# Kernel tuning notes

Measured on AMD Instinct MI355X. Metric: run time of the kernel, lower is better.

The kernel has to match this reference:

```python
import jax, jax.numpy as jnp
import numpy as np

DIM = 1024
NUM_HEADS = 16
HEAD_DIM = DIM // NUM_HEADS           # 64
WIDTH_SCALE = 0.5                      # set via configure_width in the source
CUR_HD = int(HEAD_DIM * WIDTH_SCALE)   # 32
CUR_DIM = CUR_HD * NUM_HEADS           # 512
SCALE = (HEAD_DIM ** -0.5) / (WIDTH_SCALE ** 0.5)
B, N = 2, 2048


def setup_inputs() -> dict:
    key = jax.random.key(0)
    k1, k2, k3 = jax.random.split(key, 3)
    x = jax.random.normal(k1, (B, N, DIM), dtype=jnp.float32)
    # 0.02 init keeps pre-softmax logits in a realistic range
    w_qkv = jax.random.normal(k2, (3 * DIM, DIM), dtype=jnp.float32) * 0.02
    w_proj = jax.random.normal(k3, (DIM, DIM), dtype=jnp.float32) * 0.02
    b_proj = jnp.zeros((DIM,), dtype=jnp.float32)
    return {"x": x, "w_qkv": w_qkv, "w_proj": w_proj, "b_proj": b_proj}


def reference(x, w_qkv, w_proj, b_proj):
    Bb, Nn, C = x.shape
    cq = 3 * CUR_DIM
    # dynamic-width slice of the fused QKV weight (qkv_bias=False)
    qkv = x @ w_qkv[:cq, :].T                              # (B, N, 3*CUR_DIM)
    qkv = qkv.reshape(Bb, Nn, 3, NUM_HEADS, CUR_HD).transpose(2, 0, 3, 1, 4)
    q, k, v = qkv[0], qkv[1], qkv[2]                       # (B, H, N, hd)
    attn = jax.nn.softmax(jnp.einsum('bhnd,bhmd->bhnm', q, k) * SCALE, axis=-1)
    o = jnp.einsum('bhnm,bhmd->bhnd', attn, v)             # (B, H, N, hd)
    o = o.transpose(0, 2, 1, 3).reshape(Bb, Nn, CUR_DIM)
    # proj uses only its first CUR_DIM input columns
    return o @ w_proj[:, :CUR_DIM].T + b_proj
```

## Files before the change

kernel.cpp:

```cpp
#include <hip/hip_runtime.h>

typedef __bf16 bf16;
typedef __bf16 bf16x8 __attribute__((ext_vector_type(8)));
typedef __bf16 bf16x4 __attribute__((ext_vector_type(4)));
typedef __bf16 bf16x2 __attribute__((ext_vector_type(2)));
typedef float  f32x4  __attribute__((ext_vector_type(4)));
typedef float  f32x16 __attribute__((ext_vector_type(16)));
typedef unsigned int uint32;

constexpr int DIM_  = 1024;
constexpr int NH    = 16;
constexpr int CHD   = 32;
constexpr int CDIM  = 512;
constexpr int CQ    = 1536;
constexpr int NSEQ  = 2048;
constexpr int M_    = 4096;
constexpr float ATT_SCALE = 0.17677669529663687f;
constexpr float QS_LOG2 = ATT_SCALE * 1.4426950408889634f;

__device__ inline void gload16(const bf16* g, bf16* l) {
    __builtin_amdgcn_global_load_lds((const __attribute__((address_space(1))) void*)g,
                                     (__attribute__((address_space(3))) void*)l, 16, 0, 0);
}

constexpr int NX4 = M_ * DIM_ / 4;
constexpr int NW4 = CQ * DIM_ / 4;
constexpr int NP4 = DIM_ * (CDIM / 4);
__global__ void cast_fused(const float* __restrict__ x, const float* __restrict__ wq,
                           const float* __restrict__ wp, bf16* __restrict__ xb,
                           bf16* __restrict__ wqb, bf16* __restrict__ wpb) {
    int i = blockIdx.x * blockDim.x + threadIdx.x;
    const float4* src;
    bf16x4* dst;
    if (i < NX4) {
        src = reinterpret_cast<const float4*>(x) + i;
        dst = reinterpret_cast<bf16x4*>(xb) + i;
    } else if (i < NX4 + NW4) {
        int j = i - NX4;
        src = reinterpret_cast<const float4*>(wq) + j;
        dst = reinterpret_cast<bf16x4*>(wqb) + j;
    } else {
        int j = i - (NX4 + NW4);
        int c = j >> 7, j4 = j & 127;
        src = reinterpret_cast<const float4*>(wp + c * DIM_) + j4;
        dst = reinterpret_cast<bf16x4*>(wpb + c * CDIM) + j4;
    }
    float4 v = *src;
    bf16x4 o = { (bf16)v.x, (bf16)v.y, (bf16)v.z, (bf16)v.w };
    *dst = o;
}

template<int KDIM, int MODE>
__launch_bounds__(256)
__global__ void gemm_nt(const bf16* __restrict__ A, const bf16* __restrict__ Bm,
                        bf16* __restrict__ qbo, bf16* __restrict__ kbo, bf16* __restrict__ vto,
                        float* __restrict__ Cf, const float* __restrict__ bias) {
    __shared__ __align__(16) bf16 SMEM[18432];
    bf16* As = SMEM;
    bf16* Bs = SMEM + 12288;
    const int tid = threadIdx.x;
    const int w = tid >> 6, lane = tid & 63;
    const int m0 = blockIdx.x * 128, n0 = blockIdx.y * 64;
    const int wr = (w >> 1) * 64, wc = (w & 1) * 32;
    const int lrow = lane >> 2, lk = (lane & 3) * 8;
    const int cl = lane & 15, gk8 = (lane >> 4) * 8;

    const bf16* ga = A  + (m0 + w * 16 + lrow) * KDIM + lk;
    const bf16* gb = Bm + (n0 + w * 16 + lrow) * KDIM + lk;

    constexpr int KT = KDIM / 32;

    auto stage = [&](int kt, int b) {
        gload16(ga + kt * 32,             As + b * 4096 + w * 512);
        gload16(ga + kt * 32 + 64 * KDIM, As + b * 4096 + 2048 + w * 512);
        gload16(gb + kt * 32,             Bs + b * 2048 + w * 512);
    };
    stage(0, 0);
    stage(1, 1);

    f32x4 acc[4][2] = {};

    for (int kt = 0; kt < KT; ++kt) {
        if (kt < KT - 1) asm volatile("s_waitcnt vmcnt(3)" ::: "memory");
        else             asm volatile("s_waitcnt vmcnt(0)" ::: "memory");
        __builtin_amdgcn_s_barrier();
        __builtin_amdgcn_sched_barrier(0);
        if (kt + 2 < KT) stage(kt + 2, (kt + 2) % 3);

        const bf16* as = As + (kt % 3) * 4096;
        const bf16* bs = Bs + (kt % 3) * 2048;
        bf16x8 af[4], bfr[2];
#pragma unroll
        for (int i = 0; i < 4; ++i)
            af[i]  = *reinterpret_cast<const bf16x8*>(as + (wr + i * 16 + cl) * 32 + gk8);
#pragma unroll
        for (int j = 0; j < 2; ++j)
            bfr[j] = *reinterpret_cast<const bf16x8*>(bs + (wc + j * 16 + cl) * 32 + gk8);
#pragma unroll
        for (int i = 0; i < 4; ++i)
#pragma unroll
            for (int j = 0; j < 2; ++j)
                acc[i][j] = __builtin_amdgcn_mfma_f32_16x16x32_bf16(af[i], bfr[j], acc[i][j], 0, 0, 0);
    }

    const int rg = (lane >> 4) * 4;
    if constexpr (MODE == 2) {
#pragma unroll
        for (int i = 0; i < 4; ++i)
#pragma unroll
            for (int j = 0; j < 2; ++j) {
                const int row = m0 + wr + i * 16 + rg;
                const int col = n0 + wc + j * 16 + cl;
                const float bv = bias[col];
#pragma unroll
                for (int r = 0; r < 4; ++r)
                    Cf[(row + r) * DIM_ + col] = acc[i][j][r] + bv;
            }
    } else {
        const int sec = n0 >> 9;
        if (sec == 2) {
#pragma unroll
            for (int i = 0; i < 4; ++i)
#pragma unroll
                for (int j = 0; j < 2; ++j) {
                    const int row = m0 + wr + i * 16 + rg;
                    const int col = n0 + wc + j * 16 + cl;
                    const int rem = col & 511;
                    const int h = rem >> 5, d = rem & 31;
                    const int bb = row >> 11, pos = row & 2047;
                    const int bh = bb * NH + h;
                    bf16x4 st;
#pragma unroll
                    for (int r = 0; r < 4; ++r) st[r] = (bf16)acc[i][j][r];
                    *reinterpret_cast<bf16x4*>(vto + (bh * CHD + d) * NSEQ + pos) = st;
                }
        } else {
            const float sc = sec ? 1.0f : QS_LOG2;
            __syncthreads();
#pragma unroll
            for (int i = 0; i < 4; ++i)
#pragma unroll
                for (int j = 0; j < 2; ++j)
#pragma unroll
                    for (int r = 0; r < 4; ++r)
                        SMEM[(wr + i * 16 + rg + r) * 72 + wc + j * 16 + cl] =
                            (bf16)(acc[i][j][r] * sc);
            __syncthreads();
            const int row = tid >> 1, ch = (tid & 1) * 32;
            const int m = m0 + row, bb = m >> 11, pos = m & 2047;
            const int col0 = n0 + ch;
            const int h = (col0 & 511) >> 5;
            bf16* dst = (sec ? kbo : qbo) + ((bb * NH + h) * NSEQ + pos) * CHD;
#pragma unroll
            for (int v4 = 0; v4 < 4; ++v4)
                *reinterpret_cast<bf16x8*>(dst + v4 * 8) =
                    *reinterpret_cast<const bf16x8*>(SMEM + row * 72 + ch + v4 * 8);
        }
    }
}

__device__ inline uint32 pkbf(float lo, float hi) {
    bf16x2 t = { (bf16)lo, (bf16)hi };
    return __builtin_bit_cast(uint32, t);
}

__launch_bounds__(512, 4)
__global__ void flash_kernel(const bf16* __restrict__ qb, const bf16* __restrict__ kb,
                             const bf16* __restrict__ vt, bf16* __restrict__ outb) {
    __shared__ __align__(16) char smem[32768];
    const int tid = threadIdx.x;
    const int w = tid >> 6, lane = tid & 63;
    const int lq = lane & 31, hi = lane >> 5;
    const int p = w & 3, half = w >> 2;

    const int blin = blockIdx.x;
    const int xcd = blin & 7, within = blin >> 3;
    const int head = xcd * 4 + (within >> 4);
    const int qblk = within & 15;
    const int q0 = qblk * 128 + p * 32;

    const bf16* Q = qb + head * (NSEQ * CHD);
    const bf16* K = kb + head * (NSEQ * CHD);
    const bf16* V = vt + head * (CHD * NSEQ);

    const bf16x8 qf0 = *reinterpret_cast<const bf16x8*>(Q + (q0 + lq) * CHD + hi * 8);
    const bf16x8 qf1 = *reinterpret_cast<const bf16x8*>(Q + (q0 + lq) * CHD + 16 + hi * 8);

    char* base = smem + half * 16384;
    const int sh = p >> 1, skc = p & 1;
    const bf16* srcK = K + (half * 1024 + sh * 32 + lq) * CHD + skc * 16 + hi * 8;
    const bf16* srcV = V + lq * NSEQ + half * 1024 + p * 16 + hi * 8;

    auto stage = [&](int t) {
        char* b = base + (t & 1) * 8192;
        gload16(srcK + t * 64 * CHD, (bf16*)(b + p * 1024));
        gload16(srcV + t * 64,       (bf16*)(b + 4096 + p * 1024));
    };
    stage(0);
    __syncthreads();

    f32x16 o = {};
    float rs[4] = {};
    const f32x16 zero16 = {};

    for (int t = 0; t < 16; ++t) {
        if (t < 15) stage(t + 1);
        char* buf = base + (t & 1) * 8192;
#pragma unroll
        for (int h = 0; h < 2; ++h) {
            const bf16x8 k0 = *reinterpret_cast<const bf16x8*>(buf + (h * 2 + 0) * 1024 + lane * 16);
            const bf16x8 k1 = *reinterpret_cast<const bf16x8*>(buf + (h * 2 + 1) * 1024 + lane * 16);
            __builtin_amdgcn_s_setprio(1);
            f32x16 s = __builtin_amdgcn_mfma_f32_32x32x16_bf16(k0, qf0, zero16, 0, 0, 0);
            s = __builtin_amdgcn_mfma_f32_32x32x16_bf16(k1, qf1, s, 0, 0, 0);
            __builtin_amdgcn_s_setprio(0);

#pragma unroll
            for (int r = 0; r < 16; ++r) s[r] = __builtin_amdgcn_exp2f(s[r]);
#pragma unroll
            for (int r = 0; r < 16; ++r) rs[r & 3] += s[r];

#pragma unroll
            for (int cc = 0; cc < 2; ++cc) {
                const int b8 = cc * 8;
                uint32 u0 = pkbf(s[b8 + 0], s[b8 + 1]);
                uint32 u1 = pkbf(s[b8 + 2], s[b8 + 3]);
                uint32 u2 = pkbf(s[b8 + 4], s[b8 + 5]);
                uint32 u3 = pkbf(s[b8 + 6], s[b8 + 7]);
                asm volatile("v_permlane32_swap_b32 %0, %1" : "+v"(u0), "+v"(u2));
                asm volatile("v_permlane32_swap_b32 %0, %1" : "+v"(u1), "+v"(u3));
                union { uint32 u[4]; bf16x8 v; } pb;
                pb.u[0] = u0; pb.u[1] = u1; pb.u[2] = u2; pb.u[3] = u3;
                const bf16x8 vf = *reinterpret_cast<const bf16x8*>(buf + 4096 + (h * 2 + cc) * 1024 + lane * 16);
                __builtin_amdgcn_s_setprio(1);
                o = __builtin_amdgcn_mfma_f32_32x32x16_bf16(vf, pb.v, o, 0, 0, 0);
                __builtin_amdgcn_s_setprio(0);
            }
        }
        __syncthreads();
    }

    float ls = (rs[0] + rs[1]) + (rs[2] + rs[3]);
    ls += __shfl_xor(ls, 32);

    float* Mo = (float*)(smem + p * 4608);
    float* Ml = (float*)(smem + p * 4608 + 4096);
    if (half) {
#pragma unroll
        for (int r = 0; r < 16; ++r) Mo[r * 64 + lane] = o[r];
        Ml[lane] = ls;
    }
    __syncthreads();
    if (!half) {
        const float inv = 1.f / (ls + Ml[lane]);
        const int bb = head >> 4, hh = head & 15;
        const int row = bb * NSEQ + q0 + lq;
        const int colb = hh * CHD;
#pragma unroll
        for (int rq = 0; rq < 4; ++rq) {
            bf16x4 st;
#pragma unroll
            for (int ri = 0; ri < 4; ++ri)
                st[ri] = (bf16)((o[rq * 4 + ri] + Mo[(rq * 4 + ri) * 64 + lane]) * inv);
            *reinterpret_cast<bf16x4*>(outb + row * CDIM + colb + rq * 8 + hi * 4) = st;
        }
    }
}

extern "C" void kernel_launch(void* const* d_in, const int* in_sizes, int n_in,
                              void* d_out, int out_size, void* d_ws, size_t ws_size,
                              hipStream_t stream) {
    const float* x      = (const float*)d_in[0];
    const float* w_qkv  = (const float*)d_in[1];
    const float* w_proj = (const float*)d_in[2];
    const float* b_proj = (const float*)d_in[3];
    float* out = (float*)d_out;

    char* ws = (char*)d_ws;
    bf16* xb  = (bf16*)(ws);
    bf16* wqb = (bf16*)(ws + 8388608);
    bf16* wpb = (bf16*)(ws + 11534336);
    bf16* qb  = (bf16*)(ws + 25165824);
    bf16* kb  = (bf16*)(ws + 29360128);
    bf16* vt  = (bf16*)(ws + 33554432);
    bf16* ob  = (bf16*)(ws + 37748736);

    cast_fused<<<(NX4 + NW4 + NP4) / 256, 256, 0, stream>>>(x, w_qkv, w_proj, xb, wqb, wpb);

    gemm_nt<DIM_, 1><<<dim3(32, 24), 256, 0, stream>>>(xb, wqb, qb, kb, vt, nullptr, nullptr);

    flash_kernel<<<512, 512, 0, stream>>>(qb, kb, vt, ob);

    gemm_nt<CDIM, 2><<<dim3(32, 16), 256, 0, stream>>>(ob, wpb, nullptr, nullptr, nullptr, out, b_proj);
}
```

Baseline: 72.73 us.

## Split flash KV range across four wave groups and remap GEMM LDS layout

The flash kernel now launches 1024-thread blocks where four wave groups each process a quarter of the keys (512) instead of two halves, then reduce partial outputs and row sums through LDS. This shortens the serial KV loop per wave to raise parallelism and latency hiding, at the cost of 64KB LDS per block, lower block residency, and a larger cross-group reduction. The GEMM loader is also remapped so each wave stores its MFMA fragments contiguously in LDS and reads them with lane-linear addressing, aiming to avoid LDS bank conflicts on fragment loads.

```diff
diff --git a/kernel.cpp b/kernel.cpp
--- a/kernel.cpp
+++ b/kernel.cpp
@@ -62,18 +62,17 @@
     const int w = tid >> 6, lane = tid & 63;
     const int m0 = blockIdx.x * 128, n0 = blockIdx.y * 64;
     const int wr = (w >> 1) * 64, wc = (w & 1) * 32;
-    const int lrow = lane >> 2, lk = (lane & 3) * 8;
     const int cl = lane & 15, gk8 = (lane >> 4) * 8;
 
-    const bf16* ga = A  + (m0 + w * 16 + lrow) * KDIM + lk;
-    const bf16* gb = Bm + (n0 + w * 16 + lrow) * KDIM + lk;
+    const bf16* gaA = A  + (m0 + cl) * KDIM + gk8;
+    const bf16* gbB = Bm + (n0 + cl) * KDIM + gk8;
 
     constexpr int KT = KDIM / 32;
 
     auto stage = [&](int kt, int b) {
-        gload16(ga + kt * 32,             As + b * 4096 + w * 512);
-        gload16(ga + kt * 32 + 64 * KDIM, As + b * 4096 + 2048 + w * 512);
-        gload16(gb + kt * 32,             Bs + b * 2048 + w * 512);
+        gload16(gaA + (2 * w    ) * 16 * KDIM + kt * 32, As + b * 4096 + (2 * w    ) * 512);
+        gload16(gaA + (2 * w + 1) * 16 * KDIM + kt * 32, As + b * 4096 + (2 * w + 1) * 512);
+        gload16(gbB + w * 16 * KDIM + kt * 32,           Bs + b * 2048 + w * 512);
     };
     stage(0, 0);
     stage(1, 1);
@@ -87,15 +86,15 @@
         __builtin_amdgcn_sched_barrier(0);
         if (kt + 2 < KT) stage(kt + 2, (kt + 2) % 3);
 
-        const bf16* as = As + (kt % 3) * 4096;
-        const bf16* bs = Bs + (kt % 3) * 2048;
+        const bf16* as = As + (kt % 3) * 4096 + (w >> 1) * 2048;
+        const bf16* bs = Bs + (kt % 3) * 2048 + (w & 1) * 1024;
         bf16x8 af[4], bfr[2];
 #pragma unroll
         for (int i = 0; i < 4; ++i)
-            af[i]  = *reinterpret_cast<const bf16x8*>(as + (wr + i * 16 + cl) * 32 + gk8);
+            af[i]  = *reinterpret_cast<const bf16x8*>(as + i * 512 + lane * 8);
 #pragma unroll
         for (int j = 0; j < 2; ++j)
-            bfr[j] = *reinterpret_cast<const bf16x8*>(bs + (wc + j * 16 + cl) * 32 + gk8);
+            bfr[j] = *reinterpret_cast<const bf16x8*>(bs + j * 512 + lane * 8);
 #pragma unroll
         for (int i = 0; i < 4; ++i)
 #pragma unroll
@@ -164,14 +163,14 @@
     return __builtin_bit_cast(uint32, t);
 }
 
-__launch_bounds__(512, 4)
+__launch_bounds__(1024, 8)
 __global__ void flash_kernel(const bf16* __restrict__ qb, const bf16* __restrict__ kb,
                              const bf16* __restrict__ vt, bf16* __restrict__ outb) {
-    __shared__ __align__(16) char smem[32768];
+    __shared__ __align__(16) char smem[65536];
     const int tid = threadIdx.x;
     const int w = tid >> 6, lane = tid & 63;
     const int lq = lane & 31, hi = lane >> 5;
-    const int p = w & 3, half = w >> 2;
+    const int p = w & 3, qt = w >> 2;
 
     const int blin = blockIdx.x;
     const int xcd = blin & 7, within = blin >> 3;
@@ -186,10 +185,11 @@
     const bf16x8 qf0 = *reinterpret_cast<const bf16x8*>(Q + (q0 + lq) * CHD + hi * 8);
     const bf16x8 qf1 = *reinterpret_cast<const bf16x8*>(Q + (q0 + lq) * CHD + 16 + hi * 8);
 
-    char* base = smem + half * 16384;
+    char* base = smem + qt * 16384;
+    const int kvbeg = qt * 512;
     const int sh = p >> 1, skc = p & 1;
-    const bf16* srcK = K + (half * 1024 + sh * 32 + lq) * CHD + skc * 16 + hi * 8;
-    const bf16* srcV = V + lq * NSEQ + half * 1024 + p * 16 + hi * 8;
+    const bf16* srcK = K + (kvbeg + sh * 32 + lq) * CHD + skc * 16 + hi * 8;
+    const bf16* srcV = V + lq * NSEQ + kvbeg + p * 16 + hi * 8;
 
     auto stage = [&](int t) {
         char* b = base + (t & 1) * 8192;
@@ -203,8 +203,8 @@
     float rs[4] = {};
     const f32x16 zero16 = {};
 
-    for (int t = 0; t < 16; ++t) {
-        if (t < 15) stage(t + 1);
+    for (int t = 0; t < 8; ++t) {
+        if (t < 7) stage(t + 1);
         char* buf = base + (t & 1) * 8192;
 #pragma unroll
         for (int h = 0; h < 2; ++h) {
@@ -243,16 +243,26 @@
     float ls = (rs[0] + rs[1]) + (rs[2] + rs[3]);
     ls += __shfl_xor(ls, 32);
 
-    float* Mo = (float*)(smem + p * 4608);
-    float* Ml = (float*)(smem + p * 4608 + 4096);
-    if (half) {
+    if (qt) {
+        float* Mo = (float*)(smem + p * 13824 + (qt - 1) * 4608);
+        float* Ml = (float*)(smem + p * 13824 + (qt - 1) * 4608 + 4096);
 #pragma unroll
         for (int r = 0; r < 16; ++r) Mo[r * 64 + lane] = o[r];
         Ml[lane] = ls;
     }
     __syncthreads();
-    if (!half) {
-        const float inv = 1.f / (ls + Ml[lane]);
+    if (!qt) {
+        float lt = ls;
+        f32x16 ot = o;
+#pragma unroll
+        for (int q = 0; q < 3; ++q) {
+            const float* Mo = (const float*)(smem + p * 13824 + q * 4608);
+            const float* Ml = (const float*)(smem + p * 13824 + q * 4608 + 4096);
+            lt += Ml[lane];
+#pragma unroll
+            for (int r = 0; r < 16; ++r) ot[r] += Mo[r * 64 + lane];
+        }
+        const float inv = 1.f / lt;
         const int bb = head >> 4, hh = head & 15;
         const int row = bb * NSEQ + q0 + lq;
         const int colb = hh * CHD;
@@ -261,7 +271,7 @@
             bf16x4 st;
 #pragma unroll
             for (int ri = 0; ri < 4; ++ri)
-                st[ri] = (bf16)((o[rq * 4 + ri] + Mo[(rq * 4 + ri) * 64 + lane]) * inv);
+                st[ri] = (bf16)(ot[rq * 4 + ri] * inv);
             *reinterpret_cast<bf16x4*>(outb + row * CDIM + colb + rq * 8 + hi * 4) = st;
         }
     }
@@ -289,7 +299,7 @@
 
     gemm_nt<DIM_, 1><<<dim3(32, 24), 256, 0, stream>>>(xb, wqb, qb, kb, vt, nullptr, nullptr);
 
-    flash_kernel<<<512, 512, 0, stream>>>(qb, kb, vt, ob);
+    flash_kernel<<<512, 1024, 0, stream>>>(qb, kb, vt, ob);
 
     gemm_nt<CDIM, 2><<<dim3(32, 16), 256, 0, stream>>>(ob, wpb, nullptr, nullptr, nullptr, out, b_proj);
 }
```

Measured after the change: 89.05 us. 1.22x slower.
